# Kernel optimization log

Hardware: AMD Instinct MI355X
Metric: run time of the kernel (lower is better)

The kernel has to match this reference:

```python
import jax, jax.numpy as jnp
import numpy as np

B, S, D, H, DFF = 4, 2048, 1024, 8, 4096
DH = D // H  # 128
EPS = 1e-5


def layernorm(x, gamma, beta):
    mu = jnp.mean(x, axis=-1, keepdims=True)
    var = jnp.mean(jnp.square(x - mu), axis=-1, keepdims=True)
    return (x - mu) * jax.lax.rsqrt(var + EPS) * gamma + beta


def setup_inputs() -> dict:
    key = jax.random.key(0)
    ks = jax.random.split(key, 6)
    s = 0.02
    return {
        "src": jax.random.normal(ks[0], (B, S, D), jnp.float32),
        "w_qkv": jax.random.normal(ks[1], (D, 3 * D), jnp.float32) * s,
        "w_out": jax.random.normal(ks[2], (D, D), jnp.float32) * s,
        "w1": jax.random.normal(ks[3], (D, DFF), jnp.float32) * s,
        "b1": jnp.zeros((DFF,), jnp.float32),
        "w2": jax.random.normal(ks[4], (DFF, D), jnp.float32) * s,
        "b2": jnp.zeros((D,), jnp.float32),
        "g1": jnp.ones((D,), jnp.float32),
        "beta1": jnp.zeros((D,), jnp.float32),
        "g2": jnp.ones((D,), jnp.float32),
        "beta2": jnp.zeros((D,), jnp.float32),
    }


def reference(src, w_qkv, w_out, w1, b1, w2, b2, g1, beta1, g2, beta2):
    b, s, d = src.shape
    # --- RingAttention == exact causal MHA on a single device ---
    qkv = src @ w_qkv  # [b, s, 3d]
    q, k, v = jnp.split(qkv, 3, axis=-1)
    to_heads = lambda x: x.reshape(b, s, H, DH).transpose(0, 2, 1, 3)  # [b,h,s,dh]
    q, k, v = to_heads(q), to_heads(k), to_heads(v)
    scale = 1.0 / jnp.sqrt(jnp.asarray(DH, src.dtype))
    scores = jnp.einsum('bhqd,bhkd->bhqk', q, k) * scale  # [b,h,s,s]
    causal = jnp.tril(jnp.ones((s, s), bool))
    neg = jnp.asarray(jnp.finfo(src.dtype).min, src.dtype)
    scores = jnp.where(causal, scores, neg)
    attn = jax.nn.softmax(scores, axis=-1)
    o = jnp.einsum('bhqk,bhkd->bhqd', attn, v)  # [b,h,s,dh]
    o = o.transpose(0, 2, 1, 3).reshape(b, s, d) @ w_out
    # dropout layers are identity at inference
    x = layernorm(src + o, g1, beta1)
    ff = jax.nn.relu(x @ w1 + b1) @ w2 + b2
    return layernorm(x + ff, g2, beta2)
```

## Files before the change

kernel.cpp:

```cpp
#include <hip/hip_runtime.h>

typedef unsigned short u16;
typedef __attribute__((ext_vector_type(8))) short short8;
typedef __attribute__((ext_vector_type(4))) float float4v;

#define MFMA_BF16(a, b, c) __builtin_amdgcn_mfma_f32_16x16x32_bf16((a), (b), (c), 0, 0, 0)

#define B_ 4
#define S_ 2048
#define D_ 1024
#define H_ 8
#define DH_ 128
#define DFF_ 4096
#define EPS_ 1e-5f
#define ROWS_ (B_ * S_)
#define CSCALE_ 0.12751672939502f

__device__ __forceinline__ u16 f2bf(float f) {
  union { float f; unsigned u; } x; x.f = f;
  unsigned r = x.u + 0x7fffu + ((x.u >> 16) & 1u);
  return (u16)(r >> 16);
}

typedef __attribute__((address_space(1))) const unsigned int guint;
typedef __attribute__((address_space(3))) unsigned int luint;
__device__ __forceinline__ void gl2lds16(const u16* g, u16* l) {
  __builtin_amdgcn_global_load_lds((guint*)g, (luint*)l, 16, 0, 0);
}

__global__ void cast_bf16_kernel(const float* __restrict__ in, u16* __restrict__ out, int n4) {
  int i = blockIdx.x * blockDim.x + threadIdx.x;
  int stride = gridDim.x * blockDim.x;
  for (; i < n4; i += stride) {
    float4 v = ((const float4*)in)[i];
    ushort4 u;
    u.x = f2bf(v.x); u.y = f2bf(v.y); u.z = f2bf(v.z); u.w = f2bf(v.w);
    ((ushort4*)out)[i] = u;
  }
}

__global__ void transpose_cast_kernel(const float* __restrict__ in, u16* __restrict__ out,
                                      int K, int N) {
  __shared__ float t[32][33];
  int k0 = blockIdx.x * 32, n0 = blockIdx.y * 32;
  int tx = threadIdx.x & 31, ty = threadIdx.x >> 5;
  #pragma unroll
  for (int i = 0; i < 4; ++i)
    t[ty + 8 * i][tx] = in[(size_t)(k0 + ty + 8 * i) * N + n0 + tx];
  __syncthreads();
  #pragma unroll
  for (int i = 0; i < 4; ++i)
    out[(size_t)(n0 + ty + 8 * i) * K + k0 + tx] = f2bf(t[tx][ty + 8 * i]);
}

template <int MODE>
__global__ __launch_bounds__(512, 2) void gemm256_kernel(
    const u16* __restrict__ A, const u16* __restrict__ Bt,
    const int M, const int N, const int K,
    float* __restrict__ outF, u16* __restrict__ outH, const float* __restrict__ bias,
    u16* __restrict__ qo, u16* __restrict__ ko, u16* __restrict__ vo) {
  extern __shared__ u16 smem[];
  u16* At  = smem;
  u16* Bts = smem + 2 * 256 * 64;
  const int tid = threadIdx.x;
  const int lane = tid & 63, wave = tid >> 6;
  const int quad = lane >> 4, r16 = lane & 15;
  const int halfw = wave >> 2;
  const int wn = (wave & 3) * 64;
  const int m0 = blockIdx.x * 256, n0 = blockIdx.y * 256;
  const int NT = K >> 6;

  const int rowin = wave * 8 + (lane >> 3);
  const int sc = lane & 7;
  const int shalf = rowin >> 5, srr = rowin & 31;

  const u16* Asrc[4];
  const u16* Bsrc[4];
  #pragma unroll
  for (int u = 0; u < 4; ++u) {
    const int ra = shalf * 128 + u * 32 + srr;
    Asrc[u] = A + (size_t)(m0 + ra) * K + (sc ^ (ra & 7)) * 8;
    const int rb = u * 64 + rowin;
    Bsrc[u] = Bt + (size_t)(n0 + rb) * K + (sc ^ (rb & 7)) * 8;
  }

  float4v acc[8][4];
  #pragma unroll
  for (int i = 0; i < 8; ++i)
    #pragma unroll
    for (int j = 0; j < 4; ++j) acc[i][j] = (float4v)0.0f;

#define STAGE_A(t, u) gl2lds16(Asrc[u] + (t) * 64, At  + ((t) & 1) * 16384 + (u) * 4096 + wave * 512)
#define STAGE_B(t, u) gl2lds16(Bsrc[u] + (t) * 64, Bts + ((t) & 1) * 16384 + (u) * 4096 + wave * 512)

  STAGE_B(0, 0); STAGE_B(0, 1); STAGE_B(0, 2); STAGE_B(0, 3);
  STAGE_A(0, 0); STAGE_A(0, 1); STAGE_A(0, 2); STAGE_A(0, 3);
  if (NT > 1) {
    STAGE_B(1, 0); STAGE_B(1, 1); STAGE_B(1, 2); STAGE_B(1, 3);
    STAGE_A(1, 0); STAGE_A(1, 1);
    asm volatile("s_waitcnt vmcnt(6)" ::: "memory");
  } else {
    asm volatile("s_waitcnt vmcnt(0)" ::: "memory");
  }
  __builtin_amdgcn_s_barrier();

  for (int kt = 0; kt < NT; ++kt) {
    const u16* Ab = At + (kt & 1) * 16384;
    const u16* Bb = Bts + (kt & 1) * 16384;
    short8 bfr[4][2];
    #pragma unroll
    for (int q = 0; q < 4; ++q) {
      if (q == 0) {
        #pragma unroll
        for (int j = 0; j < 4; ++j)
          #pragma unroll
          for (int s = 0; s < 2; ++s)
            bfr[j][s] = *(const short8*)(Bb + (wn + j * 16 + r16) * 64 +
                                         (((s * 4 + quad) ^ (r16 & 7)) * 8));
      }
      short8 af[2][2];
      #pragma unroll
      for (int di = 0; di < 2; ++di)
        #pragma unroll
        for (int s = 0; s < 2; ++s)
          af[di][s] = *(const short8*)(Ab + (q * 64 + halfw * 32 + di * 16 + r16) * 64 +
                                       (((s * 4 + quad) ^ (r16 & 7)) * 8));
      if (q == 0)      { if (kt + 1 < NT) { STAGE_A(kt + 1, 2); STAGE_A(kt + 1, 3); } }
      else if (q == 1) { if (kt + 2 < NT) { STAGE_B(kt + 2, 0); STAGE_B(kt + 2, 1); } }
      else if (q == 2) { if (kt + 2 < NT) { STAGE_B(kt + 2, 2); STAGE_B(kt + 2, 3); } }
      else             { if (kt + 2 < NT) { STAGE_A(kt + 2, 0); STAGE_A(kt + 2, 1); } }
      __builtin_amdgcn_s_barrier();
      asm volatile("s_waitcnt lgkmcnt(0)" ::: "memory");
      __builtin_amdgcn_s_setprio(1);
      #pragma unroll
      for (int j = 0; j < 4; ++j) {
        acc[2 * q][j]     = MFMA_BF16(af[0][0], bfr[j][0], acc[2 * q][j]);
        acc[2 * q][j]     = MFMA_BF16(af[0][1], bfr[j][1], acc[2 * q][j]);
        acc[2 * q + 1][j] = MFMA_BF16(af[1][0], bfr[j][0], acc[2 * q + 1][j]);
        acc[2 * q + 1][j] = MFMA_BF16(af[1][1], bfr[j][1], acc[2 * q + 1][j]);
      }
      __builtin_amdgcn_s_setprio(0);
      if (q == 3) {
        if (kt + 2 < NT)      { asm volatile("s_waitcnt vmcnt(6)" ::: "memory"); }
        else if (kt + 1 < NT) { asm volatile("s_waitcnt vmcnt(0)" ::: "memory"); }
      }
      __builtin_amdgcn_s_barrier();
    }
  }
#undef STAGE_A
#undef STAGE_B

  #pragma unroll
  for (int i = 0; i < 8; ++i) {
    const int rowb = m0 + halfw * 128 + i * 16 + quad * 4;
    #pragma unroll
    for (int j = 0; j < 4; ++j) {
      const int col = n0 + wn + j * 16 + r16;
      #pragma unroll
      for (int rg = 0; rg < 4; ++rg) {
        float val = acc[i][j][rg];
        const int r = rowb + rg;
        if (MODE == 2) {
          val += bias[col];
          val = fmaxf(val, 0.0f);
          outH[(size_t)r * N + col] = f2bf(val);
        } else {
          outF[(size_t)r * N + col] = val;
        }
      }
    }
  }
}

template <int MODE>
__global__ __launch_bounds__(512, 2) void gemm256x128_kernel(
    const u16* __restrict__ A, const u16* __restrict__ Bt,
    const int M, const int N, const int K,
    float* __restrict__ outF, u16* __restrict__ outH, const float* __restrict__ bias,
    u16* __restrict__ qo, u16* __restrict__ ko, u16* __restrict__ vo) {
  extern __shared__ u16 smem[];
  u16* At  = smem;
  u16* Bts = smem + 2 * 256 * 64;
  const int tid = threadIdx.x;
  const int lane = tid & 63, wave = tid >> 6;
  const int quad = lane >> 4, r16 = lane & 15;
  const int w64 = wave >> 1;
  const int wn = (wave & 1) * 64;
  const int m0 = blockIdx.x * 256, n0 = blockIdx.y * 128;
  const int NT = K >> 6;

  const int rowin = wave * 8 + (lane >> 3);
  const int sc = lane & 7;

  const u16* Asrc[4];
  const u16* Bsrc[2];
  #pragma unroll
  for (int u = 0; u < 4; ++u) {
    const int ra = ((u & 1) * 2 + (rowin >> 5)) * 64 + (u >> 1) * 32 + (rowin & 31);
    Asrc[u] = A + (size_t)(m0 + ra) * K + (sc ^ (ra & 7)) * 8;
  }
  #pragma unroll
  for (int u = 0; u < 2; ++u) {
    const int rb = u * 64 + rowin;
    Bsrc[u] = Bt + (size_t)(n0 + rb) * K + (sc ^ (rb & 7)) * 8;
  }

  float4v acc[4][4];
  #pragma unroll
  for (int i = 0; i < 4; ++i)
    #pragma unroll
    for (int j = 0; j < 4; ++j) acc[i][j] = (float4v)0.0f;

#define STAGE_A(t, u) gl2lds16(Asrc[u] + (t) * 64, At  + ((t) & 1) * 16384 + (u) * 4096 + wave * 512)
#define STAGE_B(t, u) gl2lds16(Bsrc[u] + (t) * 64, Bts + ((t) & 1) * 8192 + (u) * 4096 + wave * 512)

  STAGE_B(0, 0); STAGE_B(0, 1); STAGE_A(0, 0); STAGE_A(0, 1);
  STAGE_A(0, 2); STAGE_A(0, 3);
  STAGE_B(1, 0); STAGE_B(1, 1); STAGE_A(1, 0); STAGE_A(1, 1);
  asm volatile("s_waitcnt vmcnt(6)" ::: "memory");
  __builtin_amdgcn_s_barrier();

  for (int kt = 0; kt < NT; ++kt) {
    const u16* Ab = At + (kt & 1) * 16384;
    const u16* Bb = Bts + (kt & 1) * 8192;
    short8 bfr[4][2];
    #pragma unroll
    for (int j = 0; j < 4; ++j)
      #pragma unroll
      for (int s = 0; s < 2; ++s)
        bfr[j][s] = *(const short8*)(Bb + (wn + j * 16 + r16) * 64 +
                                     (((s * 4 + quad) ^ (r16 & 7)) * 8));
    {
      short8 af[2][2];
      #pragma unroll
      for (int di = 0; di < 2; ++di)
        #pragma unroll
        for (int s = 0; s < 2; ++s)
          af[di][s] = *(const short8*)(Ab + (w64 * 32 + di * 16 + r16) * 64 +
                                       (((s * 4 + quad) ^ (r16 & 7)) * 8));
      if (kt + 1 < NT) { STAGE_A(kt + 1, 2); STAGE_A(kt + 1, 3); }
      __builtin_amdgcn_s_barrier();
      asm volatile("s_waitcnt lgkmcnt(0)" ::: "memory");
      __builtin_amdgcn_s_setprio(1);
      #pragma unroll
      for (int j = 0; j < 4; ++j) {
        acc[0][j] = MFMA_BF16(af[0][0], bfr[j][0], acc[0][j]);
        acc[0][j] = MFMA_BF16(af[0][1], bfr[j][1], acc[0][j]);
        acc[1][j] = MFMA_BF16(af[1][0], bfr[j][0], acc[1][j]);
        acc[1][j] = MFMA_BF16(af[1][1], bfr[j][1], acc[1][j]);
      }
      __builtin_amdgcn_s_setprio(0);
      if (kt + 1 < NT) { asm volatile("s_waitcnt vmcnt(6)" ::: "memory"); }
      else             { asm volatile("s_waitcnt vmcnt(0)" ::: "memory"); }
      __builtin_amdgcn_s_barrier();
    }
    {
      short8 af[2][2];
      #pragma unroll
      for (int di = 0; di < 2; ++di)
        #pragma unroll
        for (int s = 0; s < 2; ++s)
          af[di][s] = *(const short8*)(Ab + (128 + w64 * 32 + di * 16 + r16) * 64 +
                                       (((s * 4 + quad) ^ (r16 & 7)) * 8));
      if (kt + 2 < NT) {
        STAGE_B(kt + 2, 0); STAGE_B(kt + 2, 1);
        STAGE_A(kt + 2, 0); STAGE_A(kt + 2, 1);
      }
      __builtin_amdgcn_s_barrier();
      asm volatile("s_waitcnt lgkmcnt(0)" ::: "memory");
      __builtin_amdgcn_s_setprio(1);
      #pragma unroll
      for (int j = 0; j < 4; ++j) {
        acc[2][j] = MFMA_BF16(af[0][0], bfr[j][0], acc[2][j]);
        acc[2][j] = MFMA_BF16(af[0][1], bfr[j][1], acc[2][j]);
        acc[3][j] = MFMA_BF16(af[1][0], bfr[j][0], acc[3][j]);
        acc[3][j] = MFMA_BF16(af[1][1], bfr[j][1], acc[3][j]);
      }
      __builtin_amdgcn_s_setprio(0);
      if (kt + 1 < NT) {
        if (kt + 2 < NT) { asm volatile("s_waitcnt vmcnt(6)" ::: "memory"); }
        else             { asm volatile("s_waitcnt vmcnt(2)" ::: "memory"); }
      }
      __builtin_amdgcn_s_barrier();
    }
  }
#undef STAGE_A
#undef STAGE_B

  #pragma unroll
  for (int i = 0; i < 4; ++i) {
    const int rowb = m0 + w64 * 64 + i * 16 + quad * 4;
    #pragma unroll
    for (int j = 0; j < 4; ++j) {
      const int col = n0 + wn + j * 16 + r16;
      #pragma unroll
      for (int rg = 0; rg < 4; ++rg) {
        float val = acc[i][j][rg];
        const int r = rowb + rg;
        if (MODE == 0) {
          const int part = col >> 10, cc = col & 1023;
          const int h = cc >> 7, dh = cc & 127;
          const int b = r >> 11, s = r & 2047;
          if (part == 0) {
            qo[((size_t)(b * H_ + h) * S_ + s) * DH_ + dh] = f2bf(val * CSCALE_);
          } else if (part == 1) {
            ko[((size_t)(b * H_ + h) * S_ + s) * DH_ + dh] = f2bf(val);
          } else {
            vo[((size_t)(b * H_ + h) * DH_ + dh) * S_ + s] = f2bf(val);
          }
        } else if (MODE == 1) {
          outF[(size_t)r * N + col] = val;
        } else {
          val += bias[col];
          outF[(size_t)r * N + col] = val;
        }
      }
    }
  }
}

__global__ __launch_bounds__(256) void attn_kernel(
    const u16* __restrict__ Q, const u16* __restrict__ Kg,
    const u16* __restrict__ Vtg, u16* __restrict__ O) {
  __shared__ u16 Ks[64][136];
  __shared__ u16 Vt[128][72];
  __shared__ u16 Pw[4][16][72];
  const int tid = threadIdx.x;
  const int lane = tid & 63, wave = tid >> 6;
  const int quad = lane >> 4, r16 = lane & 15;
  const int id = blockIdx.x;
  const int bh = (id & 7) * 4 + ((id >> 3) & 3);
  const int qb = 31 - (id >> 5);
  const size_t base = (size_t)bh * S_ * DH_;
  const size_t vtb = (size_t)bh * DH_ * S_;
  const int b = bh >> 3, h = bh & 7;

  const u16* kg0 = Kg + base + (size_t)(tid >> 4) * DH_ + (tid & 15) * 8;
  u16* ksl = &Ks[tid >> 4][(tid & 15) * 8];
  const u16* vg0 = Vtg + vtb + (size_t)(tid >> 3) * S_ + (tid & 7) * 8;
  u16* vtl = &Vt[tid >> 3][(tid & 7) * 8];

  short8 rk[4], rv[4];
#define LOADKV(kb_)                                                        \
  do {                                                                     \
    _Pragma("unroll")                                                      \
    for (int i_ = 0; i_ < 4; ++i_)                                         \
      rk[i_] = *(const short8*)(kg0 + (size_t)((kb_) * 64 + i_ * 16) * DH_); \
    _Pragma("unroll")                                                      \
    for (int i_ = 0; i_ < 4; ++i_)                                         \
      rv[i_] = *(const short8*)(vg0 + (size_t)i_ * 32 * S_ + (kb_) * 64);  \
  } while (0)

  const int qr = qb * 64 + wave * 16 + r16;

  short8 aq[4];
  #pragma unroll
  for (int ks = 0; ks < 4; ++ks)
    aq[ks] = *(const short8*)(Q + base + (size_t)qr * DH_ + ks * 32 + quad * 8);

  float4v acco[8];
  #pragma unroll
  for (int i = 0; i < 8; ++i) acco[i] = (float4v)0.0f;
  float m_q = -1e30f, l_q = 0.0f;

  LOADKV(0);

  for (int kb = 0; kb <= qb; ++kb) {
    __syncthreads();
    #pragma unroll
    for (int i = 0; i < 4; ++i) *(short8*)(ksl + i * 16 * 136) = rk[i];
    #pragma unroll
    for (int i = 0; i < 4; ++i) *(short8*)(vtl + i * 32 * 72) = rv[i];
    __syncthreads();
    if (kb < qb) LOADKV(kb + 1);

    float4v accs[4];
    #pragma unroll
    for (int t = 0; t < 4; ++t) accs[t] = (float4v)0.0f;
    #pragma unroll
    for (int ks = 0; ks < 4; ++ks) {
      #pragma unroll
      for (int t = 0; t < 4; ++t) {
        short8 ak = *(const short8*)&Ks[t * 16 + r16][ks * 32 + quad * 8];
        accs[t] = MFMA_BF16(ak, aq[ks], accs[t]);
      }
    }
    if (kb == qb) {
      #pragma unroll
      for (int t = 0; t < 4; ++t)
        #pragma unroll
        for (int rg = 0; rg < 4; ++rg) {
          int kc = kb * 64 + t * 16 + quad * 4 + rg;
          if (kc > qr) accs[t][rg] = -1e30f;
        }
    }
    float mv = accs[0][0];
    #pragma unroll
    for (int t = 0; t < 4; ++t)
      #pragma unroll
      for (int rg = 0; rg < 4; ++rg) mv = fmaxf(mv, accs[t][rg]);
    mv = fmaxf(mv, __shfl_xor(mv, 16));
    mv = fmaxf(mv, __shfl_xor(mv, 32));
    const bool nore = __all(mv <= m_q + 8.0f) != 0;
    const float mnew = nore ? m_q : fmaxf(m_q, mv);
    float alpha = 1.0f;
    if (!nore) alpha = __builtin_amdgcn_exp2f(m_q - mnew);
    float s0 = 0.0f;
    #pragma unroll
    for (int t = 0; t < 4; ++t)
      #pragma unroll
      for (int rg = 0; rg < 4; ++rg) {
        float p = __builtin_amdgcn_exp2f(accs[t][rg] - mnew);
        accs[t][rg] = p;
        s0 += p;
      }
    s0 += __shfl_xor(s0, 16);
    s0 += __shfl_xor(s0, 32);
    l_q = nore ? (l_q + s0) : (l_q * alpha + s0);
    m_q = mnew;

    #pragma unroll
    for (int t = 0; t < 4; ++t) {
      union { float f; unsigned u; } c0, c1, c2, c3;
      c0.f = accs[t][0]; c1.f = accs[t][1]; c2.f = accs[t][2]; c3.f = accs[t][3];
      uint2 pk;
      pk.x = ((c0.u + 0x8000u) >> 16) | ((c1.u + 0x8000u) & 0xffff0000u);
      pk.y = ((c2.u + 0x8000u) >> 16) | ((c3.u + 0x8000u) & 0xffff0000u);
      *(uint2*)&Pw[wave][r16][t * 16 + quad * 4] = pk;
    }
    if (!nore) {
      float al[4];
      #pragma unroll
      for (int rg = 0; rg < 4; ++rg) al[rg] = __shfl(alpha, quad * 4 + rg);
      #pragma unroll
      for (int nt = 0; nt < 8; ++nt)
        #pragma unroll
        for (int rg = 0; rg < 4; ++rg) acco[nt][rg] *= al[rg];
    }
    asm volatile("s_waitcnt lgkmcnt(0)" ::: "memory");
    #pragma unroll
    for (int ks2 = 0; ks2 < 2; ++ks2) {
      short8 ap = *(const short8*)&Pw[wave][r16][ks2 * 32 + quad * 8];
      #pragma unroll
      for (int nt = 0; nt < 8; ++nt) {
        short8 bv = *(const short8*)&Vt[nt * 16 + r16][ks2 * 32 + quad * 8];
        acco[nt] = MFMA_BF16(ap, bv, acco[nt]);
      }
    }
  }

  float lr[4];
  #pragma unroll
  for (int rg = 0; rg < 4; ++rg) lr[rg] = __shfl(l_q, quad * 4 + rg);
  const int sbase = qb * 64 + wave * 16 + quad * 4;
  #pragma unroll
  for (int nt = 0; nt < 8; ++nt)
    #pragma unroll
    for (int rg = 0; rg < 4; ++rg) {
      float val = acco[nt][rg] / lr[rg];
      O[((size_t)(b * S_ + sbase + rg)) * D_ + h * DH_ + nt * 16 + r16] = f2bf(val);
    }
#undef LOADKV
}

__global__ __launch_bounds__(256) void ln_kernel(
    const float* __restrict__ a, const float* __restrict__ a2,
    const float* __restrict__ res,
    const float* __restrict__ g, const float* __restrict__ be,
    float* __restrict__ xf, u16* __restrict__ xb) {
  __shared__ float red[8];
  const int row = blockIdx.x, tid = threadIdx.x;
  const float4 va = ((const float4*)(a + (size_t)row * D_))[tid];
  const float4 vr = ((const float4*)(res + (size_t)row * D_))[tid];
  float4 v;
  v.x = va.x + vr.x; v.y = va.y + vr.y; v.z = va.z + vr.z; v.w = va.w + vr.w;
  if (a2) {
    const float4 v2 = ((const float4*)(a2 + (size_t)row * D_))[tid];
    v.x += v2.x; v.y += v2.y; v.z += v2.z; v.w += v2.w;
  }
  float s = v.x + v.y + v.z + v.w;
  float q = v.x * v.x + v.y * v.y + v.z * v.z + v.w * v.w;
  #pragma unroll
  for (int m = 1; m < 64; m <<= 1) {
    s += __shfl_xor(s, m);
    q += __shfl_xor(q, m);
  }
  const int wave = tid >> 6, lane = tid & 63;
  if (lane == 0) { red[wave] = s; red[4 + wave] = q; }
  __syncthreads();
  s = red[0] + red[1] + red[2] + red[3];
  q = red[4] + red[5] + red[6] + red[7];
  const float mu = s * (1.0f / D_);
  const float var = q * (1.0f / D_) - mu * mu;
  const float inv = rsqrtf(var + EPS_);
  const float4 gg = ((const float4*)g)[tid];
  const float4 bb = ((const float4*)be)[tid];
  float4 y;
  y.x = (v.x - mu) * inv * gg.x + bb.x;
  y.y = (v.y - mu) * inv * gg.y + bb.y;
  y.z = (v.z - mu) * inv * gg.z + bb.z;
  y.w = (v.w - mu) * inv * gg.w + bb.w;
  ((float4*)(xf + (size_t)row * D_))[tid] = y;
  if (xb) {
    ushort4 u;
    u.x = f2bf(y.x); u.y = f2bf(y.y); u.z = f2bf(y.z); u.w = f2bf(y.w);
    ((ushort4*)(xb + (size_t)row * D_))[tid] = u;
  }
}

extern "C" void kernel_launch(void* const* d_in, const int* in_sizes, int n_in,
                              void* d_out, int out_size, void* d_ws, size_t ws_size,
                              hipStream_t stream) {
  const float* src   = (const float*)d_in[0];
  const float* w_qkv = (const float*)d_in[1];
  const float* w_out = (const float*)d_in[2];
  const float* w1    = (const float*)d_in[3];
  const float* b1    = (const float*)d_in[4];
  const float* w2    = (const float*)d_in[5];
  const float* b2    = (const float*)d_in[6];
  const float* g1    = (const float*)d_in[7];
  const float* be1   = (const float*)d_in[8];
  const float* g2    = (const float*)d_in[9];
  const float* be2   = (const float*)d_in[10];
  float* out = (float*)d_out;

  char* ws = (char*)d_ws;
  size_t off = 0;
  auto alloc = [&](size_t bytes) -> void* {
    void* p = ws + off;
    off += (bytes + 255) & ~(size_t)255;
    return p;
  };
  u16* src_bf = (u16*)alloc((size_t)ROWS_ * D_ * 2);
  u16* wqkvT  = (u16*)alloc((size_t)3 * D_ * D_ * 2);
  u16* woutT  = (u16*)alloc((size_t)D_ * D_ * 2);
  u16* w1T    = (u16*)alloc((size_t)DFF_ * D_ * 2);
  u16* w2T    = (u16*)alloc((size_t)D_ * DFF_ * 2);
  u16* qbuf   = (u16*)alloc((size_t)ROWS_ * D_ * 2);
  u16* kbuf   = (u16*)alloc((size_t)ROWS_ * D_ * 2);
  u16* vT     = (u16*)alloc((size_t)ROWS_ * D_ * 2);
  u16* obuf   = (u16*)alloc((size_t)ROWS_ * D_ * 2);
  float* proj = (float*)alloc((size_t)ROWS_ * D_ * 4);
  float* xf   = (float*)alloc((size_t)ROWS_ * D_ * 4);
  u16* xb     = (u16*)alloc((size_t)ROWS_ * D_ * 2);
  u16* h1     = qbuf;
  float* ff   = proj;

  const int GSMEM  = 131072;
  const int GSMEM2 = 98304;
  hipFuncSetAttribute((const void*)gemm256_kernel<2>, hipFuncAttributeMaxDynamicSharedMemorySize, GSMEM);
  hipFuncSetAttribute((const void*)gemm256x128_kernel<0>, hipFuncAttributeMaxDynamicSharedMemorySize, GSMEM2);
  hipFuncSetAttribute((const void*)gemm256x128_kernel<1>, hipFuncAttributeMaxDynamicSharedMemorySize, GSMEM2);
  hipFuncSetAttribute((const void*)gemm256x128_kernel<3>, hipFuncAttributeMaxDynamicSharedMemorySize, GSMEM2);

  cast_bf16_kernel<<<2048, 256, 0, stream>>>(src, src_bf, ROWS_ * D_ / 4);
  transpose_cast_kernel<<<dim3(D_ / 32, 3 * D_ / 32), 256, 0, stream>>>(w_qkv, wqkvT, D_, 3 * D_);
  transpose_cast_kernel<<<dim3(D_ / 32, D_ / 32), 256, 0, stream>>>(w_out, woutT, D_, D_);
  transpose_cast_kernel<<<dim3(D_ / 32, DFF_ / 32), 256, 0, stream>>>(w1, w1T, D_, DFF_);
  transpose_cast_kernel<<<dim3(DFF_ / 32, D_ / 32), 256, 0, stream>>>(w2, w2T, DFF_, D_);

  gemm256x128_kernel<0><<<dim3(ROWS_ / 256, 3 * D_ / 128), 512, GSMEM2, stream>>>(
      src_bf, wqkvT, ROWS_, 3 * D_, D_, nullptr, nullptr, nullptr, qbuf, kbuf, vT);
  attn_kernel<<<1024, 256, 0, stream>>>(qbuf, kbuf, vT, obuf);
  gemm256x128_kernel<1><<<dim3(ROWS_ / 256, D_ / 128), 512, GSMEM2, stream>>>(
      obuf, woutT, ROWS_, D_, D_, proj, nullptr, nullptr, nullptr, nullptr, nullptr);
  ln_kernel<<<ROWS_, 256, 0, stream>>>(proj, nullptr, src, g1, be1, xf, xb);
  gemm256_kernel<2><<<dim3(ROWS_ / 256, DFF_ / 256), 512, GSMEM, stream>>>(
      xb, w1T, ROWS_, DFF_, D_, nullptr, h1, b1, nullptr, nullptr, nullptr);
  gemm256x128_kernel<3><<<dim3(ROWS_ / 256, D_ / 128), 512, GSMEM2, stream>>>(
      h1, w2T, ROWS_, D_, DFF_, ff, nullptr, b2, nullptr, nullptr, nullptr);
  ln_kernel<<<ROWS_, 256, 0, stream>>>(ff, nullptr, xf, g2, be2, out, nullptr);
}
```

Measured before the change: 511.2 us.

## Pair causal query blocks per attention workgroup and stage V transpose through LDS

Each attention workgroup now processes a short and a long causal query block (qb and 31-qb), so every block does the same amount of work, and the grid shrinks from 1024 to 512 blocks. The QKV GEMM epilogue for the V part now writes the tile transposed into shared memory and stores it to global memory as coalesced 16-byte rows, replacing scattered 2-byte strided stores. The unused a2 input is removed from the layernorm kernel. Fewer blocks means each one runs longer, and any tail or occupancy imbalance is concentrated in fewer, larger blocks.

```diff
diff --git a/kernel.cpp b/kernel.cpp
--- a/kernel.cpp
+++ b/kernel.cpp
@@ -287,6 +287,34 @@
 #undef STAGE_A
 #undef STAGE_B
 
+  if (MODE == 0 && n0 >= 2 * D_) {
+    u16* vlds = smem;
+    __syncthreads();
+    #pragma unroll
+    for (int i = 0; i < 4; ++i) {
+      const int sl = w64 * 64 + i * 16 + quad * 4;
+      #pragma unroll
+      for (int j = 0; j < 4; ++j) {
+        const int dh = wn + j * 16 + r16;
+        #pragma unroll
+        for (int rg = 0; rg < 4; ++rg)
+          vlds[dh * 260 + sl + rg] = f2bf(acc[i][j][rg]);
+      }
+    }
+    __syncthreads();
+    const int b = m0 >> 11, s0 = m0 & 2047;
+    const int h = (n0 - 2 * D_) >> 7;
+    u16* vbase = vo + (size_t)(b * H_ + h) * DH_ * S_ + s0;
+    #pragma unroll
+    for (int p = 0; p < 8; ++p) {
+      const int dh = p * 16 + (tid >> 5);
+      const int ss = (tid & 31) * 8;
+      short8 v8 = *(const short8*)&vlds[dh * 260 + ss];
+      *(short8*)(vbase + (size_t)dh * S_ + ss) = v8;
+    }
+    return;
+  }
+
   #pragma unroll
   for (int i = 0; i < 4; ++i) {
     const int rowb = m0 + w64 * 64 + i * 16 + quad * 4;
@@ -303,10 +331,8 @@
           const int b = r >> 11, s = r & 2047;
           if (part == 0) {
             qo[((size_t)(b * H_ + h) * S_ + s) * DH_ + dh] = f2bf(val * CSCALE_);
-          } else if (part == 1) {
+          } else {
             ko[((size_t)(b * H_ + h) * S_ + s) * DH_ + dh] = f2bf(val);
-          } else {
-            vo[((size_t)(b * H_ + h) * DH_ + dh) * S_ + s] = f2bf(val);
           }
         } else if (MODE == 1) {
           outF[(size_t)r * N + col] = val;
@@ -329,8 +355,8 @@
   const int lane = tid & 63, wave = tid >> 6;
   const int quad = lane >> 4, r16 = lane & 15;
   const int id = blockIdx.x;
-  const int bh = (id & 7) * 4 + ((id >> 3) & 3);
-  const int qb = 31 - (id >> 5);
+  const int bh = (id & 7) * 4 + (id >> 7);
+  const int pairIdx = (id >> 3) & 15;
   const size_t base = (size_t)bh * S_ * DH_;
   const size_t vtb = (size_t)bh * DH_ * S_;
   const int b = bh >> 3, h = bh & 7;
@@ -351,121 +377,123 @@
       rv[i_] = *(const short8*)(vg0 + (size_t)i_ * 32 * S_ + (kb_) * 64);  \
   } while (0)
 
-  const int qr = qb * 64 + wave * 16 + r16;
-
-  short8 aq[4];
-  #pragma unroll
-  for (int ks = 0; ks < 4; ++ks)
-    aq[ks] = *(const short8*)(Q + base + (size_t)qr * DH_ + ks * 32 + quad * 8);
-
-  float4v acco[8];
-  #pragma unroll
-  for (int i = 0; i < 8; ++i) acco[i] = (float4v)0.0f;
-  float m_q = -1e30f, l_q = 0.0f;
-
-  LOADKV(0);
-
-  for (int kb = 0; kb <= qb; ++kb) {
-    __syncthreads();
-    #pragma unroll
-    for (int i = 0; i < 4; ++i) *(short8*)(ksl + i * 16 * 136) = rk[i];
-    #pragma unroll
-    for (int i = 0; i < 4; ++i) *(short8*)(vtl + i * 32 * 72) = rv[i];
-    __syncthreads();
-    if (kb < qb) LOADKV(kb + 1);
-
-    float4v accs[4];
-    #pragma unroll
-    for (int t = 0; t < 4; ++t) accs[t] = (float4v)0.0f;
-    #pragma unroll
-    for (int ks = 0; ks < 4; ++ks) {
+  for (int half = 0; half < 2; ++half) {
+    const int qb = (half == 0) ? pairIdx : 31 - pairIdx;
+    const int qr = qb * 64 + wave * 16 + r16;
+
+    short8 aq[4];
+    #pragma unroll
+    for (int ks = 0; ks < 4; ++ks)
+      aq[ks] = *(const short8*)(Q + base + (size_t)qr * DH_ + ks * 32 + quad * 8);
+
+    float4v acco[8];
+    #pragma unroll
+    for (int i = 0; i < 8; ++i) acco[i] = (float4v)0.0f;
+    float m_q = -1e30f, l_q = 0.0f;
+
+    LOADKV(0);
+
+    for (int kb = 0; kb <= qb; ++kb) {
+      __syncthreads();
+      #pragma unroll
+      for (int i = 0; i < 4; ++i) *(short8*)(ksl + i * 16 * 136) = rk[i];
+      #pragma unroll
+      for (int i = 0; i < 4; ++i) *(short8*)(vtl + i * 32 * 72) = rv[i];
+      __syncthreads();
+      if (kb < qb) LOADKV(kb + 1);
+
+      float4v accs[4];
+      #pragma unroll
+      for (int t = 0; t < 4; ++t) accs[t] = (float4v)0.0f;
+      #pragma unroll
+      for (int ks = 0; ks < 4; ++ks) {
+        #pragma unroll
+        for (int t = 0; t < 4; ++t) {
+          short8 ak = *(const short8*)&Ks[t * 16 + r16][ks * 32 + quad * 8];
+          accs[t] = MFMA_BF16(ak, aq[ks], accs[t]);
+        }
+      }
+      if (kb == qb) {
+        #pragma unroll
+        for (int t = 0; t < 4; ++t)
+          #pragma unroll
+          for (int rg = 0; rg < 4; ++rg) {
+            int kc = kb * 64 + t * 16 + quad * 4 + rg;
+            if (kc > qr) accs[t][rg] = -1e30f;
+          }
+      }
+      float mv = accs[0][0];
+      #pragma unroll
+      for (int t = 0; t < 4; ++t)
+        #pragma unroll
+        for (int rg = 0; rg < 4; ++rg) mv = fmaxf(mv, accs[t][rg]);
+      mv = fmaxf(mv, __shfl_xor(mv, 16));
+      mv = fmaxf(mv, __shfl_xor(mv, 32));
+      const bool nore = __all(mv <= m_q + 8.0f) != 0;
+      const float mnew = nore ? m_q : fmaxf(m_q, mv);
+      float alpha = 1.0f;
+      if (!nore) alpha = __builtin_amdgcn_exp2f(m_q - mnew);
+      float s0 = 0.0f;
+      #pragma unroll
+      for (int t = 0; t < 4; ++t)
+        #pragma unroll
+        for (int rg = 0; rg < 4; ++rg) {
+          float p = __builtin_amdgcn_exp2f(accs[t][rg] - mnew);
+          accs[t][rg] = p;
+          s0 += p;
+        }
+      s0 += __shfl_xor(s0, 16);
+      s0 += __shfl_xor(s0, 32);
+      l_q = nore ? (l_q + s0) : (l_q * alpha + s0);
+      m_q = mnew;
+
       #pragma unroll
       for (int t = 0; t < 4; ++t) {
-        short8 ak = *(const short8*)&Ks[t * 16 + r16][ks * 32 + quad * 8];
-        accs[t] = MFMA_BF16(ak, aq[ks], accs[t]);
-      }
-    }
-    if (kb == qb) {
-      #pragma unroll
-      for (int t = 0; t < 4; ++t)
-        #pragma unroll
-        for (int rg = 0; rg < 4; ++rg) {
-          int kc = kb * 64 + t * 16 + quad * 4 + rg;
-          if (kc > qr) accs[t][rg] = -1e30f;
+        union { float f; unsigned u; } c0, c1, c2, c3;
+        c0.f = accs[t][0]; c1.f = accs[t][1]; c2.f = accs[t][2]; c3.f = accs[t][3];
+        uint2 pk;
+        pk.x = ((c0.u + 0x8000u) >> 16) | ((c1.u + 0x8000u) & 0xffff0000u);
+        pk.y = ((c2.u + 0x8000u) >> 16) | ((c3.u + 0x8000u) & 0xffff0000u);
+        *(uint2*)&Pw[wave][r16][t * 16 + quad * 4] = pk;
+      }
+      if (!nore) {
+        float al[4];
+        #pragma unroll
+        for (int rg = 0; rg < 4; ++rg) al[rg] = __shfl(alpha, quad * 4 + rg);
+        #pragma unroll
+        for (int nt = 0; nt < 8; ++nt)
+          #pragma unroll
+          for (int rg = 0; rg < 4; ++rg) acco[nt][rg] *= al[rg];
+      }
+      asm volatile("s_waitcnt lgkmcnt(0)" ::: "memory");
+      #pragma unroll
+      for (int ks2 = 0; ks2 < 2; ++ks2) {
+        short8 ap = *(const short8*)&Pw[wave][r16][ks2 * 32 + quad * 8];
+        #pragma unroll
+        for (int nt = 0; nt < 8; ++nt) {
+          short8 bv = *(const short8*)&Vt[nt * 16 + r16][ks2 * 32 + quad * 8];
+          acco[nt] = MFMA_BF16(ap, bv, acco[nt]);
         }
-    }
-    float mv = accs[0][0];
-    #pragma unroll
-    for (int t = 0; t < 4; ++t)
-      #pragma unroll
-      for (int rg = 0; rg < 4; ++rg) mv = fmaxf(mv, accs[t][rg]);
-    mv = fmaxf(mv, __shfl_xor(mv, 16));
-    mv = fmaxf(mv, __shfl_xor(mv, 32));
-    const bool nore = __all(mv <= m_q + 8.0f) != 0;
-    const float mnew = nore ? m_q : fmaxf(m_q, mv);
-    float alpha = 1.0f;
-    if (!nore) alpha = __builtin_amdgcn_exp2f(m_q - mnew);
-    float s0 = 0.0f;
-    #pragma unroll
-    for (int t = 0; t < 4; ++t)
+      }
+    }
+
+    float lr[4];
+    #pragma unroll
+    for (int rg = 0; rg < 4; ++rg) lr[rg] = __shfl(l_q, quad * 4 + rg);
+    const int sbase = qb * 64 + wave * 16 + quad * 4;
+    #pragma unroll
+    for (int nt = 0; nt < 8; ++nt)
       #pragma unroll
       for (int rg = 0; rg < 4; ++rg) {
-        float p = __builtin_amdgcn_exp2f(accs[t][rg] - mnew);
-        accs[t][rg] = p;
-        s0 += p;
-      }
-    s0 += __shfl_xor(s0, 16);
-    s0 += __shfl_xor(s0, 32);
-    l_q = nore ? (l_q + s0) : (l_q * alpha + s0);
-    m_q = mnew;
-
-    #pragma unroll
-    for (int t = 0; t < 4; ++t) {
-      union { float f; unsigned u; } c0, c1, c2, c3;
-      c0.f = accs[t][0]; c1.f = accs[t][1]; c2.f = accs[t][2]; c3.f = accs[t][3];
-      uint2 pk;
-      pk.x = ((c0.u + 0x8000u) >> 16) | ((c1.u + 0x8000u) & 0xffff0000u);
-      pk.y = ((c2.u + 0x8000u) >> 16) | ((c3.u + 0x8000u) & 0xffff0000u);
-      *(uint2*)&Pw[wave][r16][t * 16 + quad * 4] = pk;
-    }
-    if (!nore) {
-      float al[4];
-      #pragma unroll
-      for (int rg = 0; rg < 4; ++rg) al[rg] = __shfl(alpha, quad * 4 + rg);
-      #pragma unroll
-      for (int nt = 0; nt < 8; ++nt)
-        #pragma unroll
-        for (int rg = 0; rg < 4; ++rg) acco[nt][rg] *= al[rg];
-    }
-    asm volatile("s_waitcnt lgkmcnt(0)" ::: "memory");
-    #pragma unroll
-    for (int ks2 = 0; ks2 < 2; ++ks2) {
-      short8 ap = *(const short8*)&Pw[wave][r16][ks2 * 32 + quad * 8];
-      #pragma unroll
-      for (int nt = 0; nt < 8; ++nt) {
-        short8 bv = *(const short8*)&Vt[nt * 16 + r16][ks2 * 32 + quad * 8];
-        acco[nt] = MFMA_BF16(ap, bv, acco[nt]);
-      }
-    }
-  }
-
-  float lr[4];
-  #pragma unroll
-  for (int rg = 0; rg < 4; ++rg) lr[rg] = __shfl(l_q, quad * 4 + rg);
-  const int sbase = qb * 64 + wave * 16 + quad * 4;
-  #pragma unroll
-  for (int nt = 0; nt < 8; ++nt)
-    #pragma unroll
-    for (int rg = 0; rg < 4; ++rg) {
-      float val = acco[nt][rg] / lr[rg];
-      O[((size_t)(b * S_ + sbase + rg)) * D_ + h * DH_ + nt * 16 + r16] = f2bf(val);
-    }
+        float val = acco[nt][rg] / lr[rg];
+        O[((size_t)(b * S_ + sbase + rg)) * D_ + h * DH_ + nt * 16 + r16] = f2bf(val);
+      }
+  }
 #undef LOADKV
 }
 
 __global__ __launch_bounds__(256) void ln_kernel(
-    const float* __restrict__ a, const float* __restrict__ a2,
-    const float* __restrict__ res,
+    const float* __restrict__ a, const float* __restrict__ res,
     const float* __restrict__ g, const float* __restrict__ be,
     float* __restrict__ xf, u16* __restrict__ xb) {
   __shared__ float red[8];
@@ -474,10 +502,6 @@
   const float4 vr = ((const float4*)(res + (size_t)row * D_))[tid];
   float4 v;
   v.x = va.x + vr.x; v.y = va.y + vr.y; v.z = va.z + vr.z; v.w = va.w + vr.w;
-  if (a2) {
-    const float4 v2 = ((const float4*)(a2 + (size_t)row * D_))[tid];
-    v.x += v2.x; v.y += v2.y; v.z += v2.z; v.w += v2.w;
-  }
   float s = v.x + v.y + v.z + v.w;
   float q = v.x * v.x + v.y * v.y + v.z * v.z + v.w * v.w;
   #pragma unroll
@@ -561,13 +585,13 @@
 
   gemm256x128_kernel<0><<<dim3(ROWS_ / 256, 3 * D_ / 128), 512, GSMEM2, stream>>>(
       src_bf, wqkvT, ROWS_, 3 * D_, D_, nullptr, nullptr, nullptr, qbuf, kbuf, vT);
-  attn_kernel<<<1024, 256, 0, stream>>>(qbuf, kbuf, vT, obuf);
+  attn_kernel<<<512, 256, 0, stream>>>(qbuf, kbuf, vT, obuf);
   gemm256x128_kernel<1><<<dim3(ROWS_ / 256, D_ / 128), 512, GSMEM2, stream>>>(
       obuf, woutT, ROWS_, D_, D_, proj, nullptr, nullptr, nullptr, nullptr, nullptr);
-  ln_kernel<<<ROWS_, 256, 0, stream>>>(proj, nullptr, src, g1, be1, xf, xb);
+  ln_kernel<<<ROWS_, 256, 0, stream>>>(proj, src, g1, be1, xf, xb);
   gemm256_kernel<2><<<dim3(ROWS_ / 256, DFF_ / 256), 512, GSMEM, stream>>>(
       xb, w1T, ROWS_, DFF_, D_, nullptr, h1, b1, nullptr, nullptr, nullptr);
   gemm256x128_kernel<3><<<dim3(ROWS_ / 256, D_ / 128), 512, GSMEM2, stream>>>(
       h1, w2T, ROWS_, D_, DFF_, ff, nullptr, b2, nullptr, nullptr, nullptr);
-  ln_kernel<<<ROWS_, 256, 0, stream>>>(ff, nullptr, xf, g2, be2, out, nullptr);
-}
+  ln_kernel<<<ROWS_, 256, 0, stream>>>(ff, xf, g2, be2, out, nullptr);
+}
```

New measurement: 480.5 us. -6.0%, faster.
